# Kernel optimization log

Measured on AMD Instinct MI355X. Metric: run time of the kernel, lower is better.

## Reference

```python
import jax, jax.numpy as jnp
import numpy as np

N, F, E, G, NNZ = 16000, 128, 256000, 512, 512000


def _hconv(xin, row, col, hw_passed, W, b, n_nodes, n_edges):
    """PyG HypergraphConv (use_attention=False), faithful to the repo's call.
    xin: [n_nodes, Fin]; row=hyper_edge[0] (graph-edge ids), col=hyper_edge[1] (hyperedge ids).
    hw_passed: [NNZ] -- the repo passes node_weight[hyper_edge[1]]; PyG then indexes it
    again by hyperedge_index[1], so the effective per-incidence weight is hw_passed[col].
    """
    xw = xin @ W                                   # lin(x), bias=False in PyG
    w = hw_passed[col]                             # [NNZ]
    D = jax.ops.segment_sum(w, row, num_segments=n_nodes)
    Dinv = jnp.where(D == 0, 0.0, 1.0 / jnp.where(D == 0, 1.0, D))
    Bdeg = jax.ops.segment_sum(jnp.ones(row.shape, xw.dtype), col, num_segments=n_edges)
    Binv = jnp.where(Bdeg == 0, 0.0, 1.0 / jnp.where(Bdeg == 0, 1.0, Bdeg))
    # node -> hyperedge: message = B[col] * xw[row], sum over col
    out_e = jax.ops.segment_sum(Binv[col][:, None] * xw[row], col, num_segments=n_edges)
    # hyperedge -> node: message = D[row] * out_e[col], sum over row
    out = jax.ops.segment_sum(Dinv[row][:, None] * out_e[col], row, num_segments=n_nodes)
    return out + b


def setup_inputs() -> dict:
    key = jax.random.key(0)
    ks = jax.random.split(key, 20)
    rn = lambda k, shape, s=0.05: jax.random.normal(k, shape, dtype=jnp.float32) * s
    return {
        "x": jax.random.normal(ks[0], (N, F), dtype=jnp.float32),
        "graph_emb": jax.random.normal(ks[1], (G, F), dtype=jnp.float32),
        "edge_index": jax.random.randint(ks[2], (2, E), 0, N),
        "edge_type": jax.random.randint(ks[3], (E,), 0, 8),
        "batch": jnp.sort(jax.random.randint(ks[4], (N,), 0, G)),
        "hyper_edge": jnp.concatenate([
            jax.random.randint(ks[5], (1, NNZ), 0, E),   # graph-edge ids
            jax.random.randint(ks[6], (1, NNZ), 0, N)],  # hyperedge ids
            axis=0),
        # HyperWeight.lin: 2F -> F -> 1
        "hw_w1": rn(ks[7], (2 * F, F)), "hw_b1": jnp.zeros((F,), jnp.float32),
        "hw_w2": rn(ks[8], (F, 1)), "hw_b2": jnp.zeros((1,), jnp.float32),
        # HypergraphConv 1: 2F -> 2F; 2: 2F -> F (lin bias=False, separate out bias)
        "c1_w": rn(ks[9], (2 * F, 2 * F)), "c1_b": jnp.zeros((2 * F,), jnp.float32),
        "c2_w": rn(ks[10], (2 * F, F)), "c2_b": jnp.zeros((F,), jnp.float32),
        # Generator.lin: 3F -> 4F -> F
        "g_w1": rn(ks[11], (3 * F, 4 * F)), "g_b1": jnp.zeros((4 * F,), jnp.float32),
        "g_w2": rn(ks[12], (4 * F, F)), "g_b2": jnp.zeros((F,), jnp.float32),
        # classifier: 2F -> F -> 1
        "cl_w1": rn(ks[13], (2 * F, F)), "cl_b1": jnp.zeros((F,), jnp.float32),
        "cl_w2": rn(ks[14], (F, 1)), "cl_b2": jnp.zeros((1,), jnp.float32),
        "attn": jnp.array([0.5, 0.5], jnp.float32),
    }


def reference(x, graph_emb, edge_index, edge_type, batch, hyper_edge,
              hw_w1, hw_b1, hw_w2, hw_b2, c1_w, c1_b, c2_w, c2_b,
              g_w1, g_b1, g_w2, g_b2, cl_w1, cl_b1, cl_w2, cl_b2, attn):
    col, row = edge_index[0], edge_index[1]
    xij0 = jnp.concatenate([x[col], x[row]], axis=-1)          # [E, 2F]
    gemb = graph_emb[batch[edge_index[0]]]                     # [E, F] (unbatch_gemb)
    proto = graph_emb[batch]                                   # [N, F]
    # HyperWeight: per-node scalar weight
    h = jax.nn.relu(jnp.concatenate([x, proto], axis=-1) @ hw_w1 + hw_b1)
    node_w = jax.nn.sigmoid(h @ hw_w2 + hw_b2)[:, 0]           # [N]
    hrow, hcol = hyper_edge[0], hyper_edge[1]
    hw_passed = node_w[hcol]                                   # [NNZ], as in repo
    er = jax.nn.sigmoid(_hconv(xij0, hrow, hcol, hw_passed, c1_w, c1_b, E, N))
    sij = jax.nn.sigmoid(_hconv(er, hrow, hcol, hw_passed, c2_w, c2_b, E, N))  # [E, F]
    # Generator.lin on [xij, gemb]
    xl = jax.nn.relu(jnp.concatenate([xij0, gemb], axis=-1) @ g_w1 + g_b1)
    xl = jax.nn.relu(xl @ g_w2 + g_b2)                         # [E, F]
    s = attn[0] * xl + attn[1] * sij
    s = jnp.concatenate([s, gemb], axis=-1)                    # [E, 2F]
    s = jax.nn.relu(s @ cl_w1 + cl_b1)
    sij_out = jax.nn.sigmoid(s @ cl_w2 + cl_b2)                # [E, 1] (eval mode)
    return sij_out
```

## Files before the change

kernel.cpp:

```cpp
#include <hip/hip_runtime.h>
#include <hip/hip_bf16.h>

#define NODES  16000
#define FDIM   128
#define EDGES  256000
#define NNZ_   512000

typedef __attribute__((ext_vector_type(8))) short bf16x8;
typedef __attribute__((ext_vector_type(4))) float f32x4;

__device__ __forceinline__ float sigmoidf_(float z) { return 1.f / (1.f + __expf(-z)); }
__device__ __forceinline__ float bflo(unsigned u) { return __uint_as_float(u << 16); }
__device__ __forceinline__ float bfhi(unsigned u) { return __uint_as_float(u & 0xffff0000u); }
__device__ __forceinline__ unsigned pack2(float lo, float hi) {
    __hip_bfloat162 h;
    h.x = __float2bfloat16(lo);
    h.y = __float2bfloat16(hi);
    return *(unsigned*)&h;
}

__global__ __launch_bounds__(128) void hyperweight_k(
    const float* __restrict__ x, const float* __restrict__ ge, const int* __restrict__ batch,
    const float* __restrict__ w1, const float* __restrict__ b1,
    const float* __restrict__ w2, const float* __restrict__ b2, float* __restrict__ node_w)
{
    __shared__ float a[8][256];
    __shared__ float red[128];
    const int t = threadIdx.x;
    const int nb = blockIdx.x * 8;
    for (int u = 0; u < 8; ++u) {
        int n = nb + u;
        a[u][t]       = x[(size_t)n * FDIM + t];
        a[u][128 + t] = ge[(size_t)batch[n] * FDIM + t];
    }
    __syncthreads();
    float acc[8] = {0,0,0,0,0,0,0,0};
    for (int k = 0; k < 256; ++k) {
        float wv = w1[k * 128 + t];
        #pragma unroll
        for (int u = 0; u < 8; ++u) acc[u] += a[u][k] * wv;
    }
    const float wv2 = w2[t];
    for (int u = 0; u < 8; ++u) {
        float h = fmaxf(acc[u] + b1[t], 0.f);
        red[t] = h * wv2;
        __syncthreads();
        for (int s2 = 64; s2 > 0; s2 >>= 1) {
            if (t < s2) red[t] += red[t + s2];
            __syncthreads();
        }
        if (t == 0) node_w[nb + u] = sigmoidf_(red[0] + b2[0]);
        __syncthreads();
    }
}

__global__ void incidence_pass(const int* __restrict__ he, const float* __restrict__ node_w,
                               float* __restrict__ D, int* __restrict__ Bcnt, int* __restrict__ rowCnt)
{
    int i = blockIdx.x * 256 + threadIdx.x;
    if (i >= NNZ_) return;
    int hr = he[i];
    int hc = he[NNZ_ + i];
    int hc2 = he[NNZ_ + hc];
    atomicAdd(&D[hr], node_w[hc2]);
    atomicAdd(&Bcnt[hc], 1);
    atomicAdd(&rowCnt[hr], 1);
}

__global__ void dinv_k(float* __restrict__ D) {
    int e = blockIdx.x * 256 + threadIdx.x;
    if (e >= EDGES) return;
    float d = D[e];
    D[e] = (d != 0.f) ? 1.f / d : 0.f;
}
__global__ void binv_k(const int* __restrict__ Bcnt, float* __restrict__ Binv) {
    int n = blockIdx.x * 256 + threadIdx.x;
    if (n >= NODES) return;
    int c = Bcnt[n];
    Binv[n] = c ? 1.f / (float)c : 0.f;
}

__global__ __launch_bounds__(1024) void reduce_chunks(const int* __restrict__ in, int* __restrict__ part, int n) {
    __shared__ int s[1024];
    int t = threadIdx.x, g = blockIdx.x * 1024 + t;
    s[t] = (g < n) ? in[g] : 0;
    __syncthreads();
    for (int d = 512; d > 0; d >>= 1) {
        if (t < d) s[t] += s[t + d];
        __syncthreads();
    }
    if (t == 0) part[blockIdx.x] = s[0];
}
__global__ __launch_bounds__(1024) void scan_sums(int* __restrict__ part, int nc) {
    __shared__ int s[1024];
    int t = threadIdx.x;
    int v = (t < nc) ? part[t] : 0;
    s[t] = v;
    __syncthreads();
    for (int d = 1; d < 1024; d <<= 1) {
        int tv = (t >= d) ? s[t - d] : 0;
        __syncthreads();
        s[t] += tv;
        __syncthreads();
    }
    if (t < nc) part[t] = s[t] - v;
}
__global__ __launch_bounds__(1024) void scan_chunks(const int* __restrict__ in, const int* __restrict__ part,
                                                    int* __restrict__ out, int n) {
    __shared__ int s[1024];
    int t = threadIdx.x, g = blockIdx.x * 1024 + t;
    int v = (g < n) ? in[g] : 0;
    s[t] = v;
    __syncthreads();
    for (int d = 1; d < 1024; d <<= 1) {
        int tv = (t >= d) ? s[t - d] : 0;
        __syncthreads();
        s[t] += tv;
        __syncthreads();
    }
    int excl = s[t] - v + part[blockIdx.x];
    if (g < n) out[g] = excl;
    if (g == n - 1) out[n] = excl + v;
}

__global__ void scatter_pass(const int* __restrict__ he, const int* __restrict__ colOff, const int* __restrict__ rowOff,
                             int* __restrict__ colCur, int* __restrict__ rowCur,
                             int* __restrict__ colList, int* __restrict__ rowList)
{
    int i = blockIdx.x * 256 + threadIdx.x;
    if (i >= NNZ_) return;
    int hr = he[i];
    int hc = he[NNZ_ + i];
    int p = colOff[hc] + atomicAdd(&colCur[hc], 1);
    colList[p] = hr;
    int q = rowOff[hr] + atomicAdd(&rowCur[hr], 1);
    rowList[q] = hc;
}

__global__ void conv_bf16(const float* __restrict__ in, __hip_bfloat16* __restrict__ out, int n) {
    int i = blockIdx.x * 256 + threadIdx.x;
    if (i < n) out[i] = __float2bfloat16(in[i]);
}
__global__ void transpose_bf16(const float* __restrict__ in, __hip_bfloat16* __restrict__ out, int K, int N) {
    int i = blockIdx.x * 256 + threadIdx.x;
    if (i >= K * N) return;
    int n = i / K, k = i - n * K;
    out[i] = __float2bfloat16(in[k * N + n]);
}

__global__ __launch_bounds__(128) void col_gather_x(
    const __hip_bfloat16* __restrict__ xb, const int* __restrict__ ei,
    const int* __restrict__ colOff, const int* __restrict__ colList, float* __restrict__ agg)
{
    int n = blockIdx.x;
    int t = threadIdx.x;
    int base = (t < 64) ? 0 : EDGES;
    int f = t & 63;
    const unsigned* x32 = (const unsigned*)xb;
    int s = colOff[n], e = colOff[n + 1];
    float vx = 0.f, vy = 0.f;
    int j = s;
    for (; j + 3 < e; j += 4) {
        int r0 = colList[j], r1 = colList[j + 1], r2 = colList[j + 2], r3 = colList[j + 3];
        unsigned q0 = x32[(size_t)ei[base + r0] * 64 + f];
        unsigned q1 = x32[(size_t)ei[base + r1] * 64 + f];
        unsigned q2 = x32[(size_t)ei[base + r2] * 64 + f];
        unsigned q3 = x32[(size_t)ei[base + r3] * 64 + f];
        vx += bflo(q0) + bflo(q1) + bflo(q2) + bflo(q3);
        vy += bfhi(q0) + bfhi(q1) + bfhi(q2) + bfhi(q3);
    }
    for (; j < e; ++j) {
        unsigned q0 = x32[(size_t)ei[base + colList[j]] * 64 + f];
        vx += bflo(q0); vy += bfhi(q0);
    }
    int ob = (t < 64) ? 0 : 128;
    float2 o = make_float2(vx, vy);
    *(float2*)(agg + (size_t)n * 256 + ob + 2 * f) = o;
}

__global__ __launch_bounds__(128) void er_k(
    const __hip_bfloat16* __restrict__ oe1, const int* __restrict__ rowOff,
    const int* __restrict__ rowList, const float* __restrict__ Dinv,
    const float* __restrict__ c1b, __hip_bfloat16* __restrict__ er)
{
    int r = blockIdx.x;
    int t = threadIdx.x;
    int s = rowOff[r], e = rowOff[r + 1];
    const unsigned* o32 = (const unsigned*)oe1;
    float vx = 0.f, vy = 0.f;
    int j = s;
    for (; j + 1 < e; j += 2) {
        unsigned q0 = o32[(size_t)rowList[j] * 128 + t];
        unsigned q1 = o32[(size_t)rowList[j + 1] * 128 + t];
        vx += bflo(q0) + bflo(q1);
        vy += bfhi(q0) + bfhi(q1);
    }
    if (j < e) {
        unsigned q0 = o32[(size_t)rowList[j] * 128 + t];
        vx += bflo(q0); vy += bfhi(q0);
    }
    float dv = Dinv[r];
    *(unsigned*)(er + (size_t)r * 256 + 2 * t) =
        pack2(sigmoidf_(dv * vx + c1b[2 * t]), sigmoidf_(dv * vy + c1b[2 * t + 1]));
}

__global__ __launch_bounds__(128) void col_agg_er(
    const __hip_bfloat16* __restrict__ er, const int* __restrict__ colOff,
    const int* __restrict__ colList, float* __restrict__ agg)
{
    int n = blockIdx.x;
    int t = threadIdx.x;
    const unsigned* e32 = (const unsigned*)er;
    int s = colOff[n], e = colOff[n + 1];
    float vx = 0.f, vy = 0.f;
    int j = s;
    for (; j + 3 < e; j += 4) {
        unsigned q0 = e32[(size_t)colList[j]     * 128 + t];
        unsigned q1 = e32[(size_t)colList[j + 1] * 128 + t];
        unsigned q2 = e32[(size_t)colList[j + 2] * 128 + t];
        unsigned q3 = e32[(size_t)colList[j + 3] * 128 + t];
        vx += bflo(q0) + bflo(q1) + bflo(q2) + bflo(q3);
        vy += bfhi(q0) + bfhi(q1) + bfhi(q2) + bfhi(q3);
    }
    for (; j < e; ++j) {
        unsigned q0 = e32[(size_t)colList[j] * 128 + t];
        vx += bflo(q0); vy += bfhi(q0);
    }
    float2 o = make_float2(vx, vy);
    *(float2*)(agg + (size_t)n * 256 + 2 * t) = o;
}

template<int K, int NN, bool OB16>
__global__ __launch_bounds__(256) void gemm_node(
    const float* __restrict__ A, const float* __restrict__ B,
    const float* __restrict__ rowscale, void* __restrict__ C)
{
    __shared__ float As[16][68];
    __shared__ float Bs[16][68];
    const int tid = threadIdx.x;
    const int m0 = blockIdx.x * 64, n0 = blockIdx.y * 64;
    const int la_k = tid & 15, la_m = tid >> 4;
    const int lb_n = tid & 63, lb_k = tid >> 6;
    const int tn = tid & 15, tm = tid >> 4;
    float acc[4][4] = {};
    for (int k0 = 0; k0 < K; k0 += 16) {
        #pragma unroll
        for (int r = 0; r < 4; ++r)
            As[la_k][la_m + 16 * r] = A[(size_t)(m0 + la_m + 16 * r) * K + k0 + la_k];
        #pragma unroll
        for (int r = 0; r < 4; ++r)
            Bs[lb_k + 4 * r][lb_n] = B[(size_t)(k0 + lb_k + 4 * r) * NN + n0 + lb_n];
        __syncthreads();
        #pragma unroll
        for (int kk = 0; kk < 16; ++kk) {
            float4 av = *(const float4*)&As[kk][tm * 4];
            float4 bv = *(const float4*)&Bs[kk][tn * 4];
            float am[4] = {av.x, av.y, av.z, av.w};
            float bn[4] = {bv.x, bv.y, bv.z, bv.w};
            #pragma unroll
            for (int i = 0; i < 4; ++i)
                #pragma unroll
                for (int j = 0; j < 4; ++j)
                    acc[i][j] += am[i] * bn[j];
        }
        __syncthreads();
    }
    #pragma unroll
    for (int i = 0; i < 4; ++i) {
        int m = m0 + tm * 4 + i;
        float rs = rowscale[m];
        if constexpr (OB16) {
            __hip_bfloat16* Cp = (__hip_bfloat16*)C + (size_t)m * NN + n0 + tn * 4;
            #pragma unroll
            for (int j = 0; j < 4; ++j) Cp[j] = __float2bfloat16(rs * acc[i][j]);
        } else {
            float4 o = make_float4(rs * acc[i][0], rs * acc[i][1], rs * acc[i][2], rs * acc[i][3]);
            *(float4*)((float*)C + (size_t)m * NN + n0 + tn * 4) = o;
        }
    }
}

__global__ void sij_k(const __hip_bfloat16* __restrict__ oe2, const int* __restrict__ rowOff,
                      const int* __restrict__ rowList, const float* __restrict__ Dinv,
                      const float* __restrict__ bias, __hip_bfloat16* __restrict__ sij)
{
    int w = (blockIdx.x * 256 + threadIdx.x) >> 6;
    int lane = threadIdx.x & 63;
    if (w >= EDGES) return;
    int s = rowOff[w], t = rowOff[w + 1];
    const unsigned* o32 = (const unsigned*)oe2;
    float ax = 0.f, ay = 0.f;
    for (int j = s; j < t; ++j) {
        unsigned q = o32[(size_t)rowList[j] * 64 + lane];
        ax += bflo(q); ay += bfhi(q);
    }
    float dv = Dinv[w];
    float2 b = *(const float2*)(bias + lane * 2);
    *(unsigned*)(sij + (size_t)w * 128 + lane * 2) =
        pack2(sigmoidf_(dv * ax + b.x), sigmoidf_(dv * ay + b.y));
}

template<int K, int LDB>
__global__ __launch_bounds__(256) void xw_mfma(
    const __hip_bfloat16* __restrict__ A, const __hip_bfloat16* __restrict__ Bt,
    __hip_bfloat16* __restrict__ dst)
{
    __shared__ __align__(16) __hip_bfloat16 As[64][40];
    __shared__ __align__(16) __hip_bfloat16 Bs[128][40];
    const int tid = threadIdx.x;
    const int m0 = blockIdx.x * 64, n0 = blockIdx.y * 128;
    const int wave = tid >> 6, lane = tid & 63;
    const int wr = wave >> 1, wc = wave & 1;
    const int srow = tid >> 2, kseg = (tid & 3) * 8;
    const int nr = tid >> 1, kb = (tid & 1) * 16;
    const int fr = lane & 15, krow = (lane >> 4) * 8, rq = lane >> 4;

    f32x4 acc[2][4] = {};
    for (int k0 = 0; k0 < K; k0 += 32) {
        *(uint4*)&As[srow][kseg] = *(const uint4*)(A + (size_t)(m0 + srow) * K + k0 + kseg);
        *(uint4*)&Bs[nr][kb]     = *(const uint4*)(Bt + (size_t)(n0 + nr) * LDB + k0 + kb);
        *(uint4*)&Bs[nr][kb + 8] = *(const uint4*)(Bt + (size_t)(n0 + nr) * LDB + k0 + kb + 8);
        __syncthreads();
        bf16x8 af[2], bf[4];
        #pragma unroll
        for (int i = 0; i < 2; ++i) af[i] = *(const bf16x8*)&As[wr * 32 + i * 16 + fr][krow];
        #pragma unroll
        for (int j = 0; j < 4; ++j) bf[j] = *(const bf16x8*)&Bs[wc * 64 + j * 16 + fr][krow];
        #pragma unroll
        for (int i = 0; i < 2; ++i)
            #pragma unroll
            for (int j = 0; j < 4; ++j)
                acc[i][j] = __builtin_amdgcn_mfma_f32_16x16x32_bf16(af[i], bf[j], acc[i][j], 0, 0, 0);
        __syncthreads();
    }
    #pragma unroll
    for (int i = 0; i < 2; ++i)
        #pragma unroll
        for (int j = 0; j < 4; ++j) {
            int col = n0 + wc * 64 + j * 16 + fr;
            #pragma unroll
            for (int r = 0; r < 4; ++r) {
                int row = m0 + wr * 32 + i * 16 + rq * 4 + r;
                dst[(size_t)row * 512 + col] = __float2bfloat16(acc[i][j][r]);
            }
        }
}

__global__ __launch_bounds__(256) void gen2_mfma(
    const __hip_bfloat16* __restrict__ xa, const __hip_bfloat16* __restrict__ xb2,
    const __hip_bfloat16* __restrict__ gc, const float* __restrict__ b1,
    const __hip_bfloat16* __restrict__ gw2t, const float* __restrict__ b2,
    const int* __restrict__ ei, const int* __restrict__ batch,
    __hip_bfloat16* __restrict__ xl2)
{
    __shared__ __align__(16) __hip_bfloat16 As[64][40];
    __shared__ __align__(16) __hip_bfloat16 Bs[128][40];
    const int tid = threadIdx.x;
    const int m0 = blockIdx.x * 64;
    const int wave = tid >> 6, lane = tid & 63;
    const int wr = wave >> 1, wc = wave & 1;
    const int srow = tid >> 2, kseg = (tid & 3) * 8;
    const int nr = tid >> 1, kb = (tid & 1) * 16;
    const int fr = lane & 15, krow = (lane >> 4) * 8, rq = lane >> 4;

    const int eg = m0 + srow;
    const int c = ei[eg];
    const __hip_bfloat16* pa = xa  + (size_t)c * 512;
    const __hip_bfloat16* pb = xb2 + (size_t)ei[EDGES + eg] * 512;
    const __hip_bfloat16* pc = gc  + (size_t)batch[c] * 512;

    f32x4 acc[2][4] = {};
    for (int k0 = 0; k0 < 512; k0 += 32) {
        int kg = k0 + kseg;
        uint4 ua = *(const uint4*)(pa + kg);
        uint4 ub = *(const uint4*)(pb + kg);
        uint4 uc = *(const uint4*)(pc + kg);
        float4 f0 = *(const float4*)(b1 + kg);
        float4 f1 = *(const float4*)(b1 + kg + 4);
        uint4 av;
        av.x = pack2(fmaxf(bflo(ua.x) + bflo(ub.x) + bflo(uc.x) + f0.x, 0.f),
                     fmaxf(bfhi(ua.x) + bfhi(ub.x) + bfhi(uc.x) + f0.y, 0.f));
        av.y = pack2(fmaxf(bflo(ua.y) + bflo(ub.y) + bflo(uc.y) + f0.z, 0.f),
                     fmaxf(bfhi(ua.y) + bfhi(ub.y) + bfhi(uc.y) + f0.w, 0.f));
        av.z = pack2(fmaxf(bflo(ua.z) + bflo(ub.z) + bflo(uc.z) + f1.x, 0.f),
                     fmaxf(bfhi(ua.z) + bfhi(ub.z) + bfhi(uc.z) + f1.y, 0.f));
        av.w = pack2(fmaxf(bflo(ua.w) + bflo(ub.w) + bflo(uc.w) + f1.z, 0.f),
                     fmaxf(bfhi(ua.w) + bfhi(ub.w) + bfhi(uc.w) + f1.w, 0.f));
        *(uint4*)&As[srow][kseg] = av;
        *(uint4*)&Bs[nr][kb]     = *(const uint4*)(gw2t + (size_t)nr * 512 + k0 + kb);
        *(uint4*)&Bs[nr][kb + 8] = *(const uint4*)(gw2t + (size_t)nr * 512 + k0 + kb + 8);
        __syncthreads();
        bf16x8 af[2], bf[4];
        #pragma unroll
        for (int i = 0; i < 2; ++i) af[i] = *(const bf16x8*)&As[wr * 32 + i * 16 + fr][krow];
        #pragma unroll
        for (int j = 0; j < 4; ++j) bf[j] = *(const bf16x8*)&Bs[wc * 64 + j * 16 + fr][krow];
        #pragma unroll
        for (int i = 0; i < 2; ++i)
            #pragma unroll
            for (int j = 0; j < 4; ++j)
                acc[i][j] = __builtin_amdgcn_mfma_f32_16x16x32_bf16(af[i], bf[j], acc[i][j], 0, 0, 0);
        __syncthreads();
    }
    #pragma unroll
    for (int i = 0; i < 2; ++i)
        #pragma unroll
        for (int j = 0; j < 4; ++j) {
            int col = wc * 64 + j * 16 + fr;
            float bc = b2[col];
            #pragma unroll
            for (int r = 0; r < 4; ++r) {
                int row = m0 + wr * 32 + i * 16 + rq * 4 + r;
                xl2[(size_t)row * 128 + col] = __float2bfloat16(fmaxf(acc[i][j][r] + bc, 0.f));
            }
        }
}

__global__ __launch_bounds__(256) void cls_mfma(
    const __hip_bfloat16* __restrict__ xl2, const __hip_bfloat16* __restrict__ sij,
    const __hip_bfloat16* __restrict__ geb, const float* __restrict__ attn,
    const __hip_bfloat16* __restrict__ clw1t, const float* __restrict__ b1,
    const float* __restrict__ w2, const float* __restrict__ b2,
    const int* __restrict__ ei, const int* __restrict__ batch,
    float* __restrict__ out)
{
    __shared__ __align__(16) __hip_bfloat16 As[64][40];
    __shared__ __align__(16) __hip_bfloat16 Bs[128][40];
    const int tid = threadIdx.x;
    const int m0 = blockIdx.x * 64;
    const int wave = tid >> 6, lane = tid & 63;
    const int srow = tid >> 2, kseg = (tid & 3) * 8;
    const int nr = tid >> 1, kb = (tid & 1) * 16;
    const int fr = lane & 15, krow = (lane >> 4) * 8, rq = lane >> 4;

    const int eg = m0 + srow;
    const int gi = batch[ei[eg]];
    const float a0 = attn[0], a1 = attn[1];

    f32x4 acc[8] = {};
    for (int k0 = 0; k0 < 256; k0 += 32) {
        int kg = k0 + kseg;
        uint4 av;
        if (kg < 128) {
            uint4 u = *(const uint4*)(xl2 + (size_t)eg * 128 + kg);
            uint4 s = *(const uint4*)(sij + (size_t)eg * 128 + kg);
            av.x = pack2(a0 * bflo(u.x) + a1 * bflo(s.x), a0 * bfhi(u.x) + a1 * bfhi(s.x));
            av.y = pack2(a0 * bflo(u.y) + a1 * bflo(s.y), a0 * bfhi(u.y) + a1 * bfhi(s.y));
            av.z = pack2(a0 * bflo(u.z) + a1 * bflo(s.z), a0 * bfhi(u.z) + a1 * bfhi(s.z));
            av.w = pack2(a0 * bflo(u.w) + a1 * bflo(s.w), a0 * bfhi(u.w) + a1 * bfhi(s.w));
        } else {
            av = *(const uint4*)(geb + (size_t)gi * 128 + kg - 128);
        }
        *(uint4*)&As[srow][kseg] = av;
        *(uint4*)&Bs[nr][kb]     = *(const uint4*)(clw1t + (size_t)nr * 256 + k0 + kb);
        *(uint4*)&Bs[nr][kb + 8] = *(const uint4*)(clw1t + (size_t)nr * 256 + k0 + kb + 8);
        __syncthreads();
        bf16x8 af = *(const bf16x8*)&As[wave * 16 + fr][krow];
        #pragma unroll
        for (int j = 0; j < 8; ++j) {
            bf16x8 bf = *(const bf16x8*)&Bs[j * 16 + fr][krow];
            acc[j] = __builtin_amdgcn_mfma_f32_16x16x32_bf16(af, bf, acc[j], 0, 0, 0);
        }
        __syncthreads();
    }
    float rsum[4] = {0.f, 0.f, 0.f, 0.f};
    #pragma unroll
    for (int j = 0; j < 8; ++j) {
        int colg = j * 16 + fr;
        float bc = b1[colg];
        float wv = w2[colg];
        #pragma unroll
        for (int r = 0; r < 4; ++r)
            rsum[r] += fmaxf(acc[j][r] + bc, 0.f) * wv;
    }
    #pragma unroll
    for (int m = 1; m < 16; m <<= 1) {
        #pragma unroll
        for (int r = 0; r < 4; ++r) rsum[r] += __shfl_xor(rsum[r], m, 64);
    }
    if (fr == 0) {
        float bb = b2[0];
        #pragma unroll
        for (int r = 0; r < 4; ++r)
            out[m0 + wave * 16 + rq * 4 + r] = sigmoidf_(rsum[r] + bb);
    }
}

extern "C" void kernel_launch(void* const* d_in, const int* in_sizes, int n_in,
                              void* d_out, int out_size, void* d_ws, size_t ws_size,
                              hipStream_t stream)
{
    const float* x     = (const float*)d_in[0];
    const float* ge    = (const float*)d_in[1];
    const int*   ei    = (const int*)d_in[2];
    const int*   batch = (const int*)d_in[4];
    const int*   he    = (const int*)d_in[5];
    const float* hw_w1 = (const float*)d_in[6];
    const float* hw_b1 = (const float*)d_in[7];
    const float* hw_w2 = (const float*)d_in[8];
    const float* hw_b2 = (const float*)d_in[9];
    const float* c1_w  = (const float*)d_in[10];
    const float* c1_b  = (const float*)d_in[11];
    const float* c2_w  = (const float*)d_in[12];
    const float* c2_b  = (const float*)d_in[13];
    const float* g_w1  = (const float*)d_in[14];
    const float* g_b1  = (const float*)d_in[15];
    const float* g_w2  = (const float*)d_in[16];
    const float* g_b2  = (const float*)d_in[17];
    const float* cl_w1 = (const float*)d_in[18];
    const float* cl_b1 = (const float*)d_in[19];
    const float* cl_w2 = (const float*)d_in[20];
    const float* cl_b2 = (const float*)d_in[21];
    const float* attn  = (const float*)d_in[22];
    float* out = (float*)d_out;

    char* ws = (char*)d_ws;
    size_t off = 0;
    auto alloc = [&](size_t nb) -> void* {
        off = (off + 255) & ~(size_t)255;
        void* p = ws + off;
        off += nb;
        return p;
    };
    float* node_w = (float*)alloc((size_t)NODES * 4);
    float* D      = (float*)alloc((size_t)EDGES * 4);
    int*   Bcnt   = (int*)  alloc((size_t)NODES * 4);
    float* Binv   = (float*)alloc((size_t)NODES * 4);
    int*   rowCnt = (int*)  alloc((size_t)EDGES * 4);
    int*   colOff = (int*)  alloc((size_t)(NODES + 1) * 4);
    int*   rowOff = (int*)  alloc((size_t)(EDGES + 1) * 4);
    int*   colCur = (int*)  alloc((size_t)NODES * 4);
    int*   rowCur = (int*)  alloc((size_t)EDGES * 4);
    int*   colList= (int*)  alloc((size_t)NNZ_ * 4);
    int*   rowList= (int*)  alloc((size_t)NNZ_ * 4);
    int*   partA  = (int*)  alloc(1024 * 4);
    int*   partB  = (int*)  alloc(1024 * 4);
    __hip_bfloat16* xb    = (__hip_bfloat16*)alloc((size_t)NODES * FDIM * 2);
    __hip_bfloat16* geb   = (__hip_bfloat16*)alloc((size_t)512 * FDIM * 2);
    __hip_bfloat16* gw1t  = (__hip_bfloat16*)alloc((size_t)512 * 384 * 2);
    __hip_bfloat16* gw2t  = (__hip_bfloat16*)alloc((size_t)128 * 512 * 2);
    __hip_bfloat16* clw1t = (__hip_bfloat16*)alloc((size_t)128 * 256 * 2);
    __hip_bfloat16* xa    = (__hip_bfloat16*)alloc((size_t)NODES * 512 * 2);
    __hip_bfloat16* xb2   = (__hip_bfloat16*)alloc((size_t)NODES * 512 * 2);
    __hip_bfloat16* gc    = (__hip_bfloat16*)alloc((size_t)512 * 512 * 2);
    float* agg  = (float*)alloc((size_t)NODES * 256 * 4);
    __hip_bfloat16* oe1b = (__hip_bfloat16*)alloc((size_t)NODES * 256 * 2);
    __hip_bfloat16* oe2  = (__hip_bfloat16*)alloc((size_t)NODES * 128 * 2);
    __hip_bfloat16* sij  = (__hip_bfloat16*)alloc((size_t)EDGES * 128 * 2);
    __hip_bfloat16* xl2  = (__hip_bfloat16*)alloc((size_t)EDGES * 128 * 2);
    __hip_bfloat16* er   = sij;

    hipMemsetAsync(D, 0, (size_t)EDGES * 4, stream);
    hipMemsetAsync(Bcnt, 0, (size_t)NODES * 4, stream);
    hipMemsetAsync(rowCnt, 0, (size_t)EDGES * 4, stream);
    hipMemsetAsync(colCur, 0, (size_t)NODES * 4, stream);
    hipMemsetAsync(rowCur, 0, (size_t)EDGES * 4, stream);

    hyperweight_k<<<NODES / 8, 128, 0, stream>>>(x, ge, batch, hw_w1, hw_b1, hw_w2, hw_b2, node_w);
    incidence_pass<<<NNZ_ / 256, 256, 0, stream>>>(he, node_w, D, Bcnt, rowCnt);
    dinv_k<<<EDGES / 256, 256, 0, stream>>>(D);
    binv_k<<<(NODES + 255) / 256, 256, 0, stream>>>(Bcnt, Binv);

    const int ncN = (NODES + 1023) / 1024;
    const int ncE = (EDGES + 1023) / 1024;
    reduce_chunks<<<ncN, 1024, 0, stream>>>(Bcnt, partA, NODES);
    scan_sums<<<1, 1024, 0, stream>>>(partA, ncN);
    scan_chunks<<<ncN, 1024, 0, stream>>>(Bcnt, partA, colOff, NODES);
    reduce_chunks<<<ncE, 1024, 0, stream>>>(rowCnt, partB, EDGES);
    scan_sums<<<1, 1024, 0, stream>>>(partB, ncE);
    scan_chunks<<<ncE, 1024, 0, stream>>>(rowCnt, partB, rowOff, EDGES);
    scatter_pass<<<NNZ_ / 256, 256, 0, stream>>>(he, colOff, rowOff, colCur, rowCur, colList, rowList);

    conv_bf16<<<(NODES * FDIM + 255) / 256, 256, 0, stream>>>(x, xb, NODES * FDIM);
    conv_bf16<<<(512 * FDIM + 255) / 256, 256, 0, stream>>>(ge, geb, 512 * FDIM);
    transpose_bf16<<<(384 * 512 + 255) / 256, 256, 0, stream>>>(g_w1, gw1t, 384, 512);
    transpose_bf16<<<(512 * 128 + 255) / 256, 256, 0, stream>>>(g_w2, gw2t, 512, 128);
    transpose_bf16<<<(256 * 128 + 255) / 256, 256, 0, stream>>>(cl_w1, clw1t, 256, 128);

    xw_mfma<128, 384><<<dim3(NODES / 64, 4), 256, 0, stream>>>(xb, gw1t, xa);
    xw_mfma<128, 384><<<dim3(NODES / 64, 4), 256, 0, stream>>>(xb, gw1t + 128, xb2);
    xw_mfma<128, 384><<<dim3(512 / 64, 4), 256, 0, stream>>>(geb, gw1t + 256, gc);

    col_gather_x<<<NODES, 128, 0, stream>>>(xb, ei, colOff, colList, agg);
    gemm_node<256, 256, true><<<dim3(NODES / 64, 4), 256, 0, stream>>>(agg, c1_w, Binv, oe1b);

    er_k<<<EDGES, 128, 0, stream>>>(oe1b, rowOff, rowList, D, c1_b, er);
    col_agg_er<<<NODES, 128, 0, stream>>>(er, colOff, colList, agg);
    gemm_node<256, 128, true><<<dim3(NODES / 64, 2), 256, 0, stream>>>(agg, c2_w, Binv, oe2);

    sij_k<<<EDGES / 4, 256, 0, stream>>>(oe2, rowOff, rowList, D, c2_b, sij);

    gen2_mfma<<<EDGES / 64, 256, 0, stream>>>(xa, xb2, gc, g_b1, gw2t, g_b2, ei, batch, xl2);

    cls_mfma<<<EDGES / 64, 256, 0, stream>>>(xl2, sij, geb, attn, clw1t, cl_b1, cl_w2, cl_b2,
                                             ei, batch, out);
}
```

Measured before the change: 810.5 us.

## Fuse sij aggregation into classifier GEMM and double-buffer gen2/cls MFMA loops

```diff
diff --git a/kernel.cpp b/kernel.cpp
--- a/kernel.cpp
+++ b/kernel.cpp
@@ -67,17 +67,16 @@
     atomicAdd(&rowCnt[hr], 1);
 }
 
-__global__ void dinv_k(float* __restrict__ D) {
-    int e = blockIdx.x * 256 + threadIdx.x;
-    if (e >= EDGES) return;
-    float d = D[e];
-    D[e] = (d != 0.f) ? 1.f / d : 0.f;
-}
-__global__ void binv_k(const int* __restrict__ Bcnt, float* __restrict__ Binv) {
-    int n = blockIdx.x * 256 + threadIdx.x;
-    if (n >= NODES) return;
-    int c = Bcnt[n];
-    Binv[n] = c ? 1.f / (float)c : 0.f;
+__global__ void inv_k(float* __restrict__ D, const int* __restrict__ Bcnt, float* __restrict__ Binv) {
+    int i = blockIdx.x * 256 + threadIdx.x;
+    if (i < EDGES) {
+        float d = D[i];
+        D[i] = (d != 0.f) ? 1.f / d : 0.f;
+    }
+    if (i < NODES) {
+        int c = Bcnt[i];
+        Binv[i] = c ? 1.f / (float)c : 0.f;
+    }
 }
 
 __global__ __launch_bounds__(1024) void reduce_chunks(const int* __restrict__ in, int* __restrict__ part, int n) {
@@ -280,26 +279,6 @@
     }
 }
 
-__global__ void sij_k(const __hip_bfloat16* __restrict__ oe2, const int* __restrict__ rowOff,
-                      const int* __restrict__ rowList, const float* __restrict__ Dinv,
-                      const float* __restrict__ bias, __hip_bfloat16* __restrict__ sij)
-{
-    int w = (blockIdx.x * 256 + threadIdx.x) >> 6;
-    int lane = threadIdx.x & 63;
-    if (w >= EDGES) return;
-    int s = rowOff[w], t = rowOff[w + 1];
-    const unsigned* o32 = (const unsigned*)oe2;
-    float ax = 0.f, ay = 0.f;
-    for (int j = s; j < t; ++j) {
-        unsigned q = o32[(size_t)rowList[j] * 64 + lane];
-        ax += bflo(q); ay += bfhi(q);
-    }
-    float dv = Dinv[w];
-    float2 b = *(const float2*)(bias + lane * 2);
-    *(unsigned*)(sij + (size_t)w * 128 + lane * 2) =
-        pack2(sigmoidf_(dv * ax + b.x), sigmoidf_(dv * ay + b.y));
-}
-
 template<int K, int LDB>
 __global__ __launch_bounds__(256) void xw_mfma(
     const __hip_bfloat16* __restrict__ A, const __hip_bfloat16* __restrict__ Bt,
@@ -353,8 +332,8 @@
     const int* __restrict__ ei, const int* __restrict__ batch,
     __hip_bfloat16* __restrict__ xl2)
 {
-    __shared__ __align__(16) __hip_bfloat16 As[64][40];
-    __shared__ __align__(16) __hip_bfloat16 Bs[128][40];
+    __shared__ __align__(16) __hip_bfloat16 As[2][64][40];
+    __shared__ __align__(16) __hip_bfloat16 Bs[2][128][40];
     const int tid = threadIdx.x;
     const int m0 = blockIdx.x * 64;
     const int wave = tid >> 6, lane = tid & 63;
@@ -369,12 +348,17 @@
     const __hip_bfloat16* pb = xb2 + (size_t)ei[EDGES + eg] * 512;
     const __hip_bfloat16* pc = gc  + (size_t)batch[c] * 512;
 
-    f32x4 acc[2][4] = {};
-    for (int k0 = 0; k0 < 512; k0 += 32) {
+    uint4 ua, ub, uc, bv0, bv1;
+    auto GLOAD = [&](int k0) {
         int kg = k0 + kseg;
-        uint4 ua = *(const uint4*)(pa + kg);
-        uint4 ub = *(const uint4*)(pb + kg);
-        uint4 uc = *(const uint4*)(pc + kg);
+        ua = *(const uint4*)(pa + kg);
+        ub = *(const uint4*)(pb + kg);
+        uc = *(const uint4*)(pc + kg);
+        bv0 = *(const uint4*)(gw2t + (size_t)nr * 512 + k0 + kb);
+        bv1 = *(const uint4*)(gw2t + (size_t)nr * 512 + k0 + kb + 8);
+    };
+    auto STORE = [&](int buf, int k0) {
+        int kg = k0 + kseg;
         float4 f0 = *(const float4*)(b1 + kg);
         float4 f1 = *(const float4*)(b1 + kg + 4);
         uint4 av;
@@ -386,20 +370,30 @@
                      fmaxf(bfhi(ua.z) + bfhi(ub.z) + bfhi(uc.z) + f1.y, 0.f));
         av.w = pack2(fmaxf(bflo(ua.w) + bflo(ub.w) + bflo(uc.w) + f1.z, 0.f),
                      fmaxf(bfhi(ua.w) + bfhi(ub.w) + bfhi(uc.w) + f1.w, 0.f));
-        *(uint4*)&As[srow][kseg] = av;
-        *(uint4*)&Bs[nr][kb]     = *(const uint4*)(gw2t + (size_t)nr * 512 + k0 + kb);
-        *(uint4*)&Bs[nr][kb + 8] = *(const uint4*)(gw2t + (size_t)nr * 512 + k0 + kb + 8);
-        __syncthreads();
+        *(uint4*)&As[buf][srow][kseg] = av;
+        *(uint4*)&Bs[buf][nr][kb]     = bv0;
+        *(uint4*)&Bs[buf][nr][kb + 8] = bv1;
+    };
+
+    GLOAD(0);
+    STORE(0, 0);
+    __syncthreads();
+
+    f32x4 acc[2][4] = {};
+    for (int it = 0; it < 16; ++it) {
+        int cur = it & 1;
+        if (it < 15) GLOAD((it + 1) * 32);
         bf16x8 af[2], bf[4];
         #pragma unroll
-        for (int i = 0; i < 2; ++i) af[i] = *(const bf16x8*)&As[wr * 32 + i * 16 + fr][krow];
-        #pragma unroll
-        for (int j = 0; j < 4; ++j) bf[j] = *(const bf16x8*)&Bs[wc * 64 + j * 16 + fr][krow];
+        for (int i = 0; i < 2; ++i) af[i] = *(const bf16x8*)&As[cur][wr * 32 + i * 16 + fr][krow];
+        #pragma unroll
+        for (int j = 0; j < 4; ++j) bf[j] = *(const bf16x8*)&Bs[cur][wc * 64 + j * 16 + fr][krow];
         #pragma unroll
         for (int i = 0; i < 2; ++i)
             #pragma unroll
             for (int j = 0; j < 4; ++j)
                 acc[i][j] = __builtin_amdgcn_mfma_f32_16x16x32_bf16(af[i], bf[j], acc[i][j], 0, 0, 0);
+        if (it < 15) STORE(cur ^ 1, (it + 1) * 32);
         __syncthreads();
     }
     #pragma unroll
@@ -417,15 +411,16 @@
 }
 
 __global__ __launch_bounds__(256) void cls_mfma(
-    const __hip_bfloat16* __restrict__ xl2, const __hip_bfloat16* __restrict__ sij,
+    const __hip_bfloat16* __restrict__ xl2, const __hip_bfloat16* __restrict__ oe2,
     const __hip_bfloat16* __restrict__ geb, const float* __restrict__ attn,
     const __hip_bfloat16* __restrict__ clw1t, const float* __restrict__ b1,
-    const float* __restrict__ w2, const float* __restrict__ b2,
+    const float* __restrict__ w2, const float* __restrict__ b2, const float* __restrict__ c2b,
     const int* __restrict__ ei, const int* __restrict__ batch,
+    const int* __restrict__ rowOff, const int* __restrict__ rowList, const float* __restrict__ Dinv,
     float* __restrict__ out)
 {
-    __shared__ __align__(16) __hip_bfloat16 As[64][40];
-    __shared__ __align__(16) __hip_bfloat16 Bs[128][40];
+    __shared__ __align__(16) __hip_bfloat16 As[2][64][40];
+    __shared__ __align__(16) __hip_bfloat16 Bs[2][128][40];
     const int tid = threadIdx.x;
     const int m0 = blockIdx.x * 64;
     const int wave = tid >> 6, lane = tid & 63;
@@ -436,31 +431,57 @@
     const int eg = m0 + srow;
     const int gi = batch[ei[eg]];
     const float a0 = attn[0], a1 = attn[1];
-
-    f32x4 acc[8] = {};
-    for (int k0 = 0; k0 < 256; k0 += 32) {
+    const int rs = rowOff[eg], re = rowOff[eg + 1];
+    const float dv = Dinv[eg];
+
+    uint4 avr, bv0, bv1;
+    auto PREP = [&](int k0) {
         int kg = k0 + kseg;
-        uint4 av;
+        bv0 = *(const uint4*)(clw1t + (size_t)nr * 256 + k0 + kb);
+        bv1 = *(const uint4*)(clw1t + (size_t)nr * 256 + k0 + kb + 8);
         if (kg < 128) {
             uint4 u = *(const uint4*)(xl2 + (size_t)eg * 128 + kg);
-            uint4 s = *(const uint4*)(sij + (size_t)eg * 128 + kg);
-            av.x = pack2(a0 * bflo(u.x) + a1 * bflo(s.x), a0 * bfhi(u.x) + a1 * bfhi(s.x));
-            av.y = pack2(a0 * bflo(u.y) + a1 * bflo(s.y), a0 * bfhi(u.y) + a1 * bfhi(s.y));
-            av.z = pack2(a0 * bflo(u.z) + a1 * bflo(s.z), a0 * bfhi(u.z) + a1 * bfhi(s.z));
-            av.w = pack2(a0 * bflo(u.w) + a1 * bflo(s.w), a0 * bfhi(u.w) + a1 * bfhi(s.w));
+            float s0 = 0.f, s1 = 0.f, s2 = 0.f, s3 = 0.f, s4 = 0.f, s5 = 0.f, s6 = 0.f, s7 = 0.f;
+            for (int q = rs; q < re; ++q) {
+                uint4 o = *(const uint4*)(oe2 + (size_t)rowList[q] * 128 + kg);
+                s0 += bflo(o.x); s1 += bfhi(o.x); s2 += bflo(o.y); s3 += bfhi(o.y);
+                s4 += bflo(o.z); s5 += bfhi(o.z); s6 += bflo(o.w); s7 += bfhi(o.w);
+            }
+            float4 c0 = *(const float4*)(c2b + kg);
+            float4 c1 = *(const float4*)(c2b + kg + 4);
+            avr.x = pack2(a0 * bflo(u.x) + a1 * sigmoidf_(dv * s0 + c0.x),
+                          a0 * bfhi(u.x) + a1 * sigmoidf_(dv * s1 + c0.y));
+            avr.y = pack2(a0 * bflo(u.y) + a1 * sigmoidf_(dv * s2 + c0.z),
+                          a0 * bfhi(u.y) + a1 * sigmoidf_(dv * s3 + c0.w));
+            avr.z = pack2(a0 * bflo(u.z) + a1 * sigmoidf_(dv * s4 + c1.x),
+                          a0 * bfhi(u.z) + a1 * sigmoidf_(dv * s5 + c1.y));
+            avr.w = pack2(a0 * bflo(u.w) + a1 * sigmoidf_(dv * s6 + c1.z),
+                          a0 * bfhi(u.w) + a1 * sigmoidf_(dv * s7 + c1.w));
         } else {
-            av = *(const uint4*)(geb + (size_t)gi * 128 + kg - 128);
+            avr = *(const uint4*)(geb + (size_t)gi * 128 + kg - 128);
         }
-        *(uint4*)&As[srow][kseg] = av;
-        *(uint4*)&Bs[nr][kb]     = *(const uint4*)(clw1t + (size_t)nr * 256 + k0 + kb);
-        *(uint4*)&Bs[nr][kb + 8] = *(const uint4*)(clw1t + (size_t)nr * 256 + k0 + kb + 8);
-        __syncthreads();
-        bf16x8 af = *(const bf16x8*)&As[wave * 16 + fr][krow];
+    };
+    auto STORE = [&](int buf) {
+        *(uint4*)&As[buf][srow][kseg] = avr;
+        *(uint4*)&Bs[buf][nr][kb]     = bv0;
+        *(uint4*)&Bs[buf][nr][kb + 8] = bv1;
+    };
+
+    PREP(0);
+    STORE(0);
+    __syncthreads();
+
+    f32x4 acc[8] = {};
+    for (int it = 0; it < 8; ++it) {
+        int cur = it & 1;
+        if (it < 7) PREP((it + 1) * 32);
+        bf16x8 af = *(const bf16x8*)&As[cur][wave * 16 + fr][krow];
         #pragma unroll
         for (int j = 0; j < 8; ++j) {
-            bf16x8 bf = *(const bf16x8*)&Bs[j * 16 + fr][krow];
+            bf16x8 bf = *(const bf16x8*)&Bs[cur][j * 16 + fr][krow];
             acc[j] = __builtin_amdgcn_mfma_f32_16x16x32_bf16(af, bf, acc[j], 0, 0, 0);
         }
+        if (it < 7) STORE(cur ^ 1);
         __syncthreads();
     }
     float rsum[4] = {0.f, 0.f, 0.f, 0.f};
@@ -522,15 +543,16 @@
         off += nb;
         return p;
     };
-    float* node_w = (float*)alloc((size_t)NODES * 4);
     float* D      = (float*)alloc((size_t)EDGES * 4);
     int*   Bcnt   = (int*)  alloc((size_t)NODES * 4);
+    int*   rowCnt = (int*)  alloc((size_t)EDGES * 4);
+    int*   colCur = (int*)  alloc((size_t)NODES * 4);
+    int*   rowCur = (int*)  alloc((size_t)EDGES * 4);
+    size_t zero_end = off;
+    float* node_w = (float*)alloc((size_t)NODES * 4);
     float* Binv   = (float*)alloc((size_t)NODES * 4);
-    int*   rowCnt = (int*)  alloc((size_t)EDGES * 4);
     int*   colOff = (int*)  alloc((size_t)(NODES + 1) * 4);
     int*   rowOff = (int*)  alloc((size_t)(EDGES + 1) * 4);
-    int*   colCur = (int*)  alloc((size_t)NODES * 4);
-    int*   rowCur = (int*)  alloc((size_t)EDGES * 4);
     int*   colList= (int*)  alloc((size_t)NNZ_ * 4);
     int*   rowList= (int*)  alloc((size_t)NNZ_ * 4);
     int*   partA  = (int*)  alloc(1024 * 4);
@@ -546,20 +568,14 @@
     float* agg  = (float*)alloc((size_t)NODES * 256 * 4);
     __hip_bfloat16* oe1b = (__hip_bfloat16*)alloc((size_t)NODES * 256 * 2);
     __hip_bfloat16* oe2  = (__hip_bfloat16*)alloc((size_t)NODES * 128 * 2);
-    __hip_bfloat16* sij  = (__hip_bfloat16*)alloc((size_t)EDGES * 128 * 2);
-    __hip_bfloat16* xl2  = (__hip_bfloat16*)alloc((size_t)EDGES * 128 * 2);
-    __hip_bfloat16* er   = sij;
-
-    hipMemsetAsync(D, 0, (size_t)EDGES * 4, stream);
-    hipMemsetAsync(Bcnt, 0, (size_t)NODES * 4, stream);
-    hipMemsetAsync(rowCnt, 0, (size_t)EDGES * 4, stream);
-    hipMemsetAsync(colCur, 0, (size_t)NODES * 4, stream);
-    hipMemsetAsync(rowCur, 0, (size_t)EDGES * 4, stream);
+    __hip_bfloat16* er   = (__hip_bfloat16*)alloc((size_t)EDGES * 256 * 2);
+    __hip_bfloat16* xl2  = er;
+
+    hipMemsetAsync(D, 0, zero_end, stream);
 
     hyperweight_k<<<NODES / 8, 128, 0, stream>>>(x, ge, batch, hw_w1, hw_b1, hw_w2, hw_b2, node_w);
     incidence_pass<<<NNZ_ / 256, 256, 0, stream>>>(he, node_w, D, Bcnt, rowCnt);
-    dinv_k<<<EDGES / 256, 256, 0, stream>>>(D);
-    binv_k<<<(NODES + 255) / 256, 256, 0, stream>>>(Bcnt, Binv);
+    inv_k<<<EDGES / 256, 256, 0, stream>>>(D, Bcnt, Binv);
 
     const int ncN = (NODES + 1023) / 1024;
     const int ncE = (EDGES + 1023) / 1024;
@@ -588,10 +604,8 @@
     col_agg_er<<<NODES, 128, 0, stream>>>(er, colOff, colList, agg);
     gemm_node<256, 128, true><<<dim3(NODES / 64, 2), 256, 0, stream>>>(agg, c2_w, Binv, oe2);
 
-    sij_k<<<EDGES / 4, 256, 0, stream>>>(oe2, rowOff, rowList, D, c2_b, sij);
-
     gen2_mfma<<<EDGES / 64, 256, 0, stream>>>(xa, xb2, gc, g_b1, gw2t, g_b2, ei, batch, xl2);
 
-    cls_mfma<<<EDGES / 64, 256, 0, stream>>>(xl2, sij, geb, attn, clw1t, cl_b1, cl_w2, cl_b2,
-                                             ei, batch, out);
-}
+    cls_mfma<<<EDGES / 64, 256, 0, stream>>>(xl2, oe2, geb, attn, clw1t, cl_b1, cl_w2, cl_b2,
+                                             c2_b, ei, batch, rowOff, rowList, D, out);
+}
```

Result: faster. 770.5 us (-4.9%).
